# Kernel tuning notes

Hardware: AMD Instinct MI355X
Metric: run time of the kernel (lower is better)

Reference implementation:

```python
import jax, jax.numpy as jnp
import numpy as np

LAYERS = 20
BLOCK = 10
K = 2
LC = 16   # layer channels
SC = 32   # skip channels
AC = 64   # aggregate channels
CLASSES = 256


def causal_conv(x, W, b, dilation):
    # x: (B, Cin, N), W: (Cout, Cin, K) -> (B, Cout, N), left-padded (causal)
    pad = dilation * (W.shape[-1] - 1)
    y = jax.lax.conv_general_dilated(
        x, W, window_strides=(1,), padding=[(pad, 0)],
        rhs_dilation=(dilation,), dimension_numbers=('NCH', 'OIH', 'NCH'))
    return y + b[None, :, None]


def conv1x1(x, W, b):
    # (B,Cin,N) x (Cout,Cin,1) -> (B,Cout,N)
    return jnp.einsum('bcn,oc->bon', x, W[:, :, 0]) + b[None, :, None]


def setup_inputs() -> dict:
    key = jax.random.key(0)
    ks = jax.random.split(key, 16)
    B, N = 8, 32768
    x_int = jax.random.randint(ks[0], (B, N), 0, 32768, dtype=jnp.int32)
    s = 0.1
    return {
        'x_int': x_int,
        'W0': jax.random.normal(ks[1], (LC, 1, K), jnp.float32) * s,
        'b0': jnp.zeros((LC,), jnp.float32),
        'Wf': jax.random.normal(ks[2], (LAYERS - 1, LC, LC, K), jnp.float32) * s,
        'bf': jnp.zeros((LAYERS - 1, LC), jnp.float32),
        'Wg': jax.random.normal(ks[3], (LAYERS - 1, LC, LC, K), jnp.float32) * s,
        'bg': jnp.zeros((LAYERS - 1, LC), jnp.float32),
        'Wskip': jax.random.normal(ks[4], (LAYERS - 1, SC, LC, 1), jnp.float32) * s,
        'bskip': jnp.zeros((LAYERS - 1, SC), jnp.float32),
        'Wagg': jax.random.normal(ks[5], (AC, SC, 1), jnp.float32) * s,
        'bagg': jnp.zeros((AC,), jnp.float32),
        'Wout': jax.random.normal(ks[6], (CLASSES, AC, 1), jnp.float32) * s,
        'bout': jnp.zeros((CLASSES,), jnp.float32),
    }


def reference(x_int, W0, b0, Wf, bf, Wg, bg, Wskip, bskip, Wagg, bagg, Wout, bout):
    B, N = x_int.shape
    # build_layer_input: normalize, shift right by one sample (causal teacher forcing)
    x = x_int.astype(jnp.float32) / (65536.0 / 2.0)
    x = jnp.concatenate([jnp.zeros((B, 1), jnp.float32), x[:, :-1]], axis=1)
    h = x[:, None, :]                                  # (B, 1, N)

    # layer 0: plain causal conv 1 -> 16 channels; residual broadcasts (B,1,N)+(B,16,N)
    out0 = causal_conv(h, W0, b0, 1)
    h = h + out0                                       # (B, 16, N)

    skip_acc = jnp.zeros((B, SC, N), jnp.float32)
    for i in range(LAYERS - 1):
        d = 2 ** ((i + 1) % BLOCK)
        f = jnp.tanh(causal_conv(h, Wf[i], bf[i], d))
        g = jax.nn.sigmoid(causal_conv(h, Wg[i], bg[i], d))
        skip_acc = skip_acc + conv1x1(h, Wskip[i], bskip[i])  # skip taps layer INPUT (per source)
        h = h + f * g                                  # residual

    agg = conv1x1(jax.nn.relu(skip_acc), Wagg, bagg)   # (B, 64, N)
    logits = conv1x1(jax.nn.relu(agg), Wout, bout)     # (B, 256, N)
    # full-length sequences -> mask is all ones; log-softmax over channel dim
    return jax.nn.log_softmax(logits, axis=1)
```

## Files before the change

### kernel.cpp

```cpp
#include <hip/hip_runtime.h>
#include <math.h>
#include <stdint.h>

#define NPOS  32768
#define LOG2N 15
#define BATCH 8
#define TOTAL (BATCH * NPOS)
#define HE    ((size_t)16 * TOTAL)
#define HFE   ((size_t)16 * TOTAL)

typedef __attribute__((ext_vector_type(8))) short    short8v;
typedef __attribute__((ext_vector_type(8))) _Float16 half8v;
typedef __attribute__((ext_vector_type(4))) float    f32x4;

__device__ __forceinline__ float fast_tanh(float x) {
    float t = __expf(-2.f * x);
    return fmaf(2.f, __builtin_amdgcn_rcpf(1.f + t), -1.f);
}
__device__ __forceinline__ float fast_sigmoid(float x) {
    return __builtin_amdgcn_rcpf(1.f + __expf(-x));
}
__device__ __forceinline__ unsigned short bf16rne(float x) {
    unsigned u = __float_as_uint(x);
    u = (u + 0x7fffu + ((u >> 16) & 1u)) >> 16;
    return (unsigned short)u;
}
__device__ __forceinline__ unsigned short f16bits(float x) {
    union { _Float16 h; unsigned short u; } cv;
    cv.h = (_Float16)x;
    return cv.u;
}


__global__ __launch_bounds__(256) void init_f16(
    const int* __restrict__ x_int, const float* __restrict__ W0,
    const float* __restrict__ b0, _Float16* __restrict__ H0)
{
    int t0 = (blockIdx.x * 256 + threadIdx.x) * 2;
    int n0 = t0 & (NPOS - 1);
    const float sc = 1.f / 32768.f;
    float xs0  = (n0 >= 1) ? (float)x_int[t0 - 1] * sc : 0.f;
    float xs1  = (float)x_int[t0] * sc;
    float xsp0 = (n0 >= 2) ? (float)x_int[t0 - 2] * sc : 0.f;
    float xsp1 = xs0;

    half8v o[4];
#pragma unroll
    for (int c = 0; c < 16; ++c) {
        float a = xs0 + W0[c * 2 + 0] * xsp0 + W0[c * 2 + 1] * xs0 + b0[c];
        float b = xs1 + W0[c * 2 + 0] * xsp1 + W0[c * 2 + 1] * xs1 + b0[c];
        o[c >> 3][c & 7]       = (_Float16)a;
        o[2 + (c >> 3)][c & 7] = (_Float16)b;
    }
    half8v* op = (half8v*)(H0 + (size_t)t0 * 16);
    op[0] = o[0]; op[1] = o[1]; op[2] = o[2]; op[3] = o[3];
}

__global__ __launch_bounds__(256, 4) void layer_mfma(
    const _Float16* __restrict__ hIn, _Float16* __restrict__ hOut,
    const float* __restrict__ wf, const float* __restrict__ bfv,
    const float* __restrict__ wg, const float* __restrict__ bgv,
    int d)
{
    const int tid  = threadIdx.x;
    const int lane = tid & 63;
    const int wv   = tid >> 6;
    const int lr   = lane & 15;
    const int lg   = lane >> 4;

    const int koff = (lg & 1) * 8;
    const int sel  = lg >> 1;
    half8v af, ag;
#pragma unroll
    for (int j = 0; j < 8; ++j) {
        af[j] = (_Float16)wf[(lr * 16 + koff + j) * 2 + sel];
        ag[j] = (_Float16)wg[(lr * 16 + koff + j) * 2 + sel];
    }
    f32x4 cf0, cg0;
#pragma unroll
    for (int r = 0; r < 4; ++r) {
        cf0[r] = bfv[lg * 4 + r];
        cg0[r] = bgv[lg * 4 + r];
    }

    const int waveBase = blockIdx.x * 256 + wv * 64;

#pragma unroll
    for (int nt = 0; nt < 4; ++nt) {
        int t = waveBase + nt * 16 + lr;
        int n = t & (NPOS - 1);

        half8v bfr;
        if (sel == 0) {
            bool v = (n >= d);
            const half8v* p = (const half8v*)(hIn + (size_t)(v ? (t - d) : t) * 16 + koff);
            half8v x = *p;
            if (!v) {
#pragma unroll
                for (int j = 0; j < 8; ++j) x[j] = (_Float16)0.f;
            }
            bfr = x;
        } else {
            bfr = *(const half8v*)(hIn + (size_t)t * 16 + koff);
        }

        f32x4 fAcc = __builtin_amdgcn_mfma_f32_16x16x32_f16(af, bfr, cf0, 0, 0, 0);
        f32x4 gAcc = __builtin_amdgcn_mfma_f32_16x16x32_f16(ag, bfr, cg0, 0, 0, 0);

        const _Float16* hold = hIn + (size_t)t * 16 + lg * 4;
        unsigned pk0, pk1;
        {
            float v0 = fmaf(fast_tanh(fAcc[0]), fast_sigmoid(gAcc[0]), (float)hold[0]);
            float v1 = fmaf(fast_tanh(fAcc[1]), fast_sigmoid(gAcc[1]), (float)hold[1]);
            float v2 = fmaf(fast_tanh(fAcc[2]), fast_sigmoid(gAcc[2]), (float)hold[2]);
            float v3 = fmaf(fast_tanh(fAcc[3]), fast_sigmoid(gAcc[3]), (float)hold[3]);
            pk0 = (unsigned)f16bits(v0) | ((unsigned)f16bits(v1) << 16);
            pk1 = (unsigned)f16bits(v2) | ((unsigned)f16bits(v3) << 16);
        }
        *(uint2*)(hOut + (size_t)t * 16 + lg * 4) = make_uint2(pk0, pk1);
    }
}

__global__ __launch_bounds__(256, 2) void final_f16(
    const _Float16* __restrict__ Hf,
    const float* __restrict__ Wsk,  const float* __restrict__ bskv,
    const float* __restrict__ Wagg, const float* __restrict__ bagg,
    const float* __restrict__ Wout, const float* __restrict__ bout,
    float* __restrict__ out)
{
    __shared__ float sv_lds[64][33];
    __shared__ unsigned short agg_bu[64 * 64];
    __shared__ float red_m[64][5];
    __shared__ float red_s[64][5];
    __shared__ float bsum[32];

    int tid  = threadIdx.x;
    int lane = tid & 63;
    int w    = tid >> 6;
    int posG = blockIdx.x * 64;
    int b    = posG >> LOG2N;
    int nb   = posG & (NPOS - 1);

    int lr = lane & 15;
    int lg = lane >> 4;

    if (tid < 32) {
        float s = 0.f;
#pragma unroll 1
        for (int i = 0; i < 19; ++i) s += bskv[i * 32 + tid];
        bsum[tid] = s;
    }

    int posGlob = posG + w * 16 + lr;

    f32x4 dsk0 = {0.f, 0.f, 0.f, 0.f};
    f32x4 dsk1 = {0.f, 0.f, 0.f, 0.f};

#pragma unroll
    for (int kt = 0; kt < 10; ++kt) {
        int i   = kt * 2 + (lg >> 1);
        int ic0 = (lg & 1) * 8;
        half8v bfr = {0, 0, 0, 0, 0, 0, 0, 0};
        half8v af0 = {0, 0, 0, 0, 0, 0, 0, 0};
        half8v af1 = {0, 0, 0, 0, 0, 0, 0, 0};
        if (i < 19) {
            bfr = *(const half8v*)(Hf + (size_t)i * HFE + (size_t)posGlob * 16 + ic0);

            const float4* wp0 = (const float4*)(Wsk + (size_t)i * 512 + (0 * 16 + lr) * 16 + ic0);
            const float4* wp1 = (const float4*)(Wsk + (size_t)i * 512 + (1 * 16 + lr) * 16 + ic0);
            float4 a0 = wp0[0], a1 = wp0[1];
            float4 c0v = wp1[0], c1v = wp1[1];
            af0[0] = (_Float16)a0.x; af0[1] = (_Float16)a0.y;
            af0[2] = (_Float16)a0.z; af0[3] = (_Float16)a0.w;
            af0[4] = (_Float16)a1.x; af0[5] = (_Float16)a1.y;
            af0[6] = (_Float16)a1.z; af0[7] = (_Float16)a1.w;
            af1[0] = (_Float16)c0v.x; af1[1] = (_Float16)c0v.y;
            af1[2] = (_Float16)c0v.z; af1[3] = (_Float16)c0v.w;
            af1[4] = (_Float16)c1v.x; af1[5] = (_Float16)c1v.y;
            af1[6] = (_Float16)c1v.z; af1[7] = (_Float16)c1v.w;
        }
        dsk0 = __builtin_amdgcn_mfma_f32_16x16x32_f16(af0, bfr, dsk0, 0, 0, 0);
        dsk1 = __builtin_amdgcn_mfma_f32_16x16x32_f16(af1, bfr, dsk1, 0, 0, 0);
    }

    __syncthreads();

    {
        int posL = w * 16 + lr;
#pragma unroll
        for (int r = 0; r < 4; ++r) {
            int sc0 = 0 * 16 + lg * 4 + r;
            int sc1 = 1 * 16 + lg * 4 + r;
            sv_lds[posL][sc0] = fmaxf(dsk0[r] + bsum[sc0], 0.f);
            sv_lds[posL][sc1] = fmaxf(dsk1[r] + bsum[sc1], 0.f);
        }
    }
    __syncthreads();

    {
        float sv[32];
#pragma unroll
        for (int sch = 0; sch < 32; ++sch) sv[sch] = sv_lds[lane][sch];

        float r16[16];
#pragma unroll
        for (int a = 0; a < 16; ++a) {
            int ac = w * 16 + a;
            float acc = bagg[ac];
#pragma unroll
            for (int sch = 0; sch < 32; ++sch)
                acc = fmaf(Wagg[ac * 32 + sch], sv[sch], acc);
            r16[a] = fmaxf(acc, 0.f);
        }
#pragma unroll
        for (int q = 0; q < 8; ++q) {
            unsigned pk = (unsigned)f16bits(r16[2 * q]) |
                          ((unsigned)f16bits(r16[2 * q + 1]) << 16);
            int icbyte = (w * 16 + 2 * q) * 2;
            int addr   = lane * 128 + (icbyte ^ ((lane & 7) << 4));
            *(unsigned*)(&agg_bu[addr >> 1]) = pk;
        }
    }
    __syncthreads();

    int c0 = w * 64;
    half8v afr[4][2];
#pragma unroll
    for (int ct = 0; ct < 4; ++ct) {
#pragma unroll
        for (int kf = 0; kf < 2; ++kf) {
            int cls = c0 + ct * 16 + lr;
            int k0  = kf * 32 + lg * 8;
            const float4* wp = (const float4*)(Wout + (size_t)cls * 64 + k0);
            float4 w0 = wp[0], w1 = wp[1];
            half8v af;
            af[0] = (_Float16)w0.x; af[1] = (_Float16)w0.y;
            af[2] = (_Float16)w0.z; af[3] = (_Float16)w0.w;
            af[4] = (_Float16)w1.x; af[5] = (_Float16)w1.y;
            af[6] = (_Float16)w1.z; af[7] = (_Float16)w1.w;
            afr[ct][kf] = af;
        }
    }

    f32x4 acc[4][4];
#pragma unroll
    for (int pt = 0; pt < 4; ++pt) {
        int pos = pt * 16 + lr;
        int sw  = (pos & 7) << 4;
        const half8v* bp0 = (const half8v*)(&agg_bu[(pos * 128 + ((0 * 64 + lg * 16) ^ sw)) >> 1]);
        const half8v* bp1 = (const half8v*)(&agg_bu[(pos * 128 + ((1 * 64 + lg * 16) ^ sw)) >> 1]);
        half8v bf0 = *bp0;
        half8v bf1 = *bp1;
#pragma unroll
        for (int ct = 0; ct < 4; ++ct) {
            f32x4 c;
#pragma unroll
            for (int r = 0; r < 4; ++r) c[r] = bout[c0 + ct * 16 + lg * 4 + r];
            c = __builtin_amdgcn_mfma_f32_16x16x32_f16(afr[ct][0], bf0, c, 0, 0, 0);
            c = __builtin_amdgcn_mfma_f32_16x16x32_f16(afr[ct][1], bf1, c, 0, 0, 0);
            acc[pt][ct] = c;
        }
    }

#pragma unroll
    for (int pt = 0; pt < 4; ++pt) {
        float m = -1e30f;
#pragma unroll
        for (int ct = 0; ct < 4; ++ct)
#pragma unroll
            for (int r = 0; r < 4; ++r) m = fmaxf(m, acc[pt][ct][r]);
        m = fmaxf(m, __shfl_xor(m, 16));
        m = fmaxf(m, __shfl_xor(m, 32));
        float s = 0.f;
#pragma unroll
        for (int ct = 0; ct < 4; ++ct)
#pragma unroll
            for (int r = 0; r < 4; ++r) s += __expf(acc[pt][ct][r] - m);
        s += __shfl_xor(s, 16);
        s += __shfl_xor(s, 32);
        int pos = pt * 16 + lr;
        red_m[pos][w] = m;
        red_s[pos][w] = s;
    }
    __syncthreads();

#pragma unroll
    for (int pt = 0; pt < 4; ++pt) {
        int pos = pt * 16 + lr;
        float M = fmaxf(fmaxf(red_m[pos][0], red_m[pos][1]),
                        fmaxf(red_m[pos][2], red_m[pos][3]));
        float S = 0.f;
#pragma unroll
        for (int k = 0; k < 4; ++k) S += red_s[pos][k] * __expf(red_m[pos][k] - M);
        float logZ = M + __logf(S);

        int n = nb + pos;
#pragma unroll
        for (int ct = 0; ct < 4; ++ct) {
#pragma unroll
            for (int r = 0; r < 4; ++r) {
                int cls = c0 + ct * 16 + lg * 4 + r;
                out[((size_t)(b * 256 + cls)) * NPOS + n] = acc[pt][ct][r] - logZ;
            }
        }
    }
}

__global__ __launch_bounds__(256) void init_kernel2(
    const int* __restrict__ x_int, const float* __restrict__ W0,
    const float* __restrict__ b0, float* __restrict__ h)
{
    int t0 = (blockIdx.x * 256 + threadIdx.x) * 2;
    int n0 = t0 & (NPOS - 1);
    const float sc = 1.f / 32768.f;
    float xs0  = (n0 >= 1) ? (float)x_int[t0 - 1] * sc : 0.f;
    float xs1  = (float)x_int[t0] * sc;
    float xsp0 = (n0 >= 2) ? (float)x_int[t0 - 2] * sc : 0.f;
    float xsp1 = xs0;
#pragma unroll
    for (int c = 0; c < 16; ++c) {
        float2 o;
        o.x = xs0 + W0[c * 2 + 0] * xsp0 + W0[c * 2 + 1] * xs0 + b0[c];
        o.y = xs1 + W0[c * 2 + 0] * xsp1 + W0[c * 2 + 1] * xs1 + b0[c];
        *(float2*)(h + (size_t)c * TOTAL + t0) = o;
    }
}

__global__ __launch_bounds__(256, 2) void layer_kernel2(
    const float* __restrict__ hIn, float* __restrict__ hOut,
    float* __restrict__ skip,
    const float* __restrict__ wf, const float* __restrict__ bfv,
    const float* __restrict__ wg, const float* __restrict__ bgv,
    const float* __restrict__ wsk, const float* __restrict__ bskv,
    int d, int firstLayer)
{
    int t0 = (blockIdx.x * 256 + threadIdx.x) * 2;
    int n0 = t0 & (NPOS - 1);

    float2 hc[16], hp[16];
#pragma unroll
    for (int ic = 0; ic < 16; ++ic)
        hc[ic] = *(const float2*)(hIn + (size_t)ic * TOTAL + t0);

    if (d == 1) {
        bool v = (n0 >= 1);
        int tm = v ? (t0 - 1) : t0;
#pragma unroll
        for (int ic = 0; ic < 16; ++ic) {
            float x = hIn[(size_t)ic * TOTAL + tm];
            hp[ic].x = v ? x : 0.f;
            hp[ic].y = hc[ic].x;
        }
    } else {
        bool v = (n0 >= d);
        int tm = v ? (t0 - d) : t0;
#pragma unroll
        for (int ic = 0; ic < 16; ++ic) {
            float2 x = *(const float2*)(hIn + (size_t)ic * TOTAL + tm);
            hp[ic].x = v ? x.x : 0.f;
            hp[ic].y = v ? x.y : 0.f;
        }
    }

    float2 fa[16], ga[16];
#pragma unroll
    for (int c = 0; c < 16; ++c) {
        fa[c].x = fa[c].y = bfv[c];
        ga[c].x = ga[c].y = bgv[c];
    }
#pragma unroll
    for (int c = 0; c < 16; ++c) {
#pragma unroll
        for (int ic = 0; ic < 16; ++ic) {
            float wf0 = wf[(c * 16 + ic) * 2 + 0];
            float wf1 = wf[(c * 16 + ic) * 2 + 1];
            float wg0 = wg[(c * 16 + ic) * 2 + 0];
            float wg1 = wg[(c * 16 + ic) * 2 + 1];
            fa[c].x = fmaf(wf0, hp[ic].x, fa[c].x);
            fa[c].x = fmaf(wf1, hc[ic].x, fa[c].x);
            fa[c].y = fmaf(wf0, hp[ic].y, fa[c].y);
            fa[c].y = fmaf(wf1, hc[ic].y, fa[c].y);
            ga[c].x = fmaf(wg0, hp[ic].x, ga[c].x);
            ga[c].x = fmaf(wg1, hc[ic].x, ga[c].x);
            ga[c].y = fmaf(wg0, hp[ic].y, ga[c].y);
            ga[c].y = fmaf(wg1, hc[ic].y, ga[c].y);
        }
    }

#pragma unroll
    for (int c = 0; c < 16; ++c) {
        float2 o;
        o.x = fmaf(fast_tanh(fa[c].x), fast_sigmoid(ga[c].x), hc[c].x);
        o.y = fmaf(fast_tanh(fa[c].y), fast_sigmoid(ga[c].y), hc[c].y);
        *(float2*)(hOut + (size_t)c * TOTAL + t0) = o;
    }

#pragma unroll
    for (int sch = 0; sch < 32; ++sch) {
        float2 acc;
        acc.x = acc.y = bskv[sch];
#pragma unroll
        for (int ic = 0; ic < 16; ++ic) {
            float wv = wsk[sch * 16 + ic];
            acc.x = fmaf(wv, hc[ic].x, acc.x);
            acc.y = fmaf(wv, hc[ic].y, acc.y);
        }
        float* sp = skip + (size_t)sch * TOTAL + t0;
        if (firstLayer) {
            *(float2*)sp = acc;
        } else {
            float2 old = *(const float2*)sp;
            acc.x += old.x; acc.y += old.y;
            *(float2*)sp = acc;
        }
    }
}

__global__ __launch_bounds__(256, 2) void final_kernel(
    const float* __restrict__ skip,
    const float* __restrict__ Wagg, const float* __restrict__ bagg,
    const float* __restrict__ Wout, const float* __restrict__ bout,
    float* __restrict__ out)
{
    __shared__ unsigned short agg_bu[64 * 64];
    __shared__ float red_m[64][5];
    __shared__ float red_s[64][5];

    int tid  = threadIdx.x;
    int lane = tid & 63;
    int w    = tid >> 6;
    int posG = blockIdx.x * 64;
    int b    = posG >> LOG2N;
    int nb   = posG & (NPOS - 1);

    {
        int pos = posG + lane;
        float sv[32];
#pragma unroll
        for (int sch = 0; sch < 32; ++sch)
            sv[sch] = fmaxf(skip[(size_t)sch * TOTAL + pos], 0.f);

        float r16[16];
#pragma unroll
        for (int a = 0; a < 16; ++a) {
            int ac = w * 16 + a;
            float acc = bagg[ac];
#pragma unroll
            for (int sch = 0; sch < 32; ++sch)
                acc = fmaf(Wagg[ac * 32 + sch], sv[sch], acc);
            r16[a] = fmaxf(acc, 0.f);
        }
#pragma unroll
        for (int q = 0; q < 8; ++q) {
            unsigned pk = (unsigned)bf16rne(r16[2 * q]) |
                          ((unsigned)bf16rne(r16[2 * q + 1]) << 16);
            int icbyte = (w * 16 + 2 * q) * 2;
            int addr   = lane * 128 + (icbyte ^ ((lane & 7) << 4));
            *(unsigned*)(&agg_bu[addr >> 1]) = pk;
        }
    }
    __syncthreads();

    int lr = lane & 15;
    int lg = lane >> 4;
    int c0 = w * 64;
    short8v afr[4][2];
#pragma unroll
    for (int ct = 0; ct < 4; ++ct) {
#pragma unroll
        for (int kf = 0; kf < 2; ++kf) {
            int cls = c0 + ct * 16 + lr;
            int k0  = kf * 32 + lg * 8;
            const float4* wp = (const float4*)(Wout + (size_t)cls * 64 + k0);
            float4 w0 = wp[0], w1 = wp[1];
            short8v af;
            af[0] = (short)bf16rne(w0.x); af[1] = (short)bf16rne(w0.y);
            af[2] = (short)bf16rne(w0.z); af[3] = (short)bf16rne(w0.w);
            af[4] = (short)bf16rne(w1.x); af[5] = (short)bf16rne(w1.y);
            af[6] = (short)bf16rne(w1.z); af[7] = (short)bf16rne(w1.w);
            afr[ct][kf] = af;
        }
    }

    f32x4 acc[4][4];
#pragma unroll
    for (int pt = 0; pt < 4; ++pt) {
        int pos = pt * 16 + lr;
        int sw  = (pos & 7) << 4;
        const short8v* bp0 = (const short8v*)(&agg_bu[(pos * 128 + ((0 * 64 + lg * 16) ^ sw)) >> 1]);
        const short8v* bp1 = (const short8v*)(&agg_bu[(pos * 128 + ((1 * 64 + lg * 16) ^ sw)) >> 1]);
        short8v bf0 = *bp0;
        short8v bf1 = *bp1;
#pragma unroll
        for (int ct = 0; ct < 4; ++ct) {
            f32x4 c;
#pragma unroll
            for (int r = 0; r < 4; ++r) c[r] = bout[c0 + ct * 16 + lg * 4 + r];
            c = __builtin_amdgcn_mfma_f32_16x16x32_bf16(afr[ct][0], bf0, c, 0, 0, 0);
            c = __builtin_amdgcn_mfma_f32_16x16x32_bf16(afr[ct][1], bf1, c, 0, 0, 0);
            acc[pt][ct] = c;
        }
    }

#pragma unroll
    for (int pt = 0; pt < 4; ++pt) {
        float m = -1e30f;
#pragma unroll
        for (int ct = 0; ct < 4; ++ct)
#pragma unroll
            for (int r = 0; r < 4; ++r) m = fmaxf(m, acc[pt][ct][r]);
        m = fmaxf(m, __shfl_xor(m, 16));
        m = fmaxf(m, __shfl_xor(m, 32));
        float s = 0.f;
#pragma unroll
        for (int ct = 0; ct < 4; ++ct)
#pragma unroll
            for (int r = 0; r < 4; ++r) s += __expf(acc[pt][ct][r] - m);
        s += __shfl_xor(s, 16);
        s += __shfl_xor(s, 32);
        int pos = pt * 16 + lr;
        red_m[pos][w] = m;
        red_s[pos][w] = s;
    }
    __syncthreads();

#pragma unroll
    for (int pt = 0; pt < 4; ++pt) {
        int pos = pt * 16 + lr;
        float M = fmaxf(fmaxf(red_m[pos][0], red_m[pos][1]),
                        fmaxf(red_m[pos][2], red_m[pos][3]));
        float S = 0.f;
#pragma unroll
        for (int k = 0; k < 4; ++k) S += red_s[pos][k] * __expf(red_m[pos][k] - M);
        float logZ = M + __logf(S);

        int n = nb + pos;
#pragma unroll
        for (int ct = 0; ct < 4; ++ct) {
#pragma unroll
            for (int r = 0; r < 4; ++r) {
                int cls = c0 + ct * 16 + lg * 4 + r;
                out[((size_t)(b * 256 + cls)) * NPOS + n] = acc[pt][ct][r] - logZ;
            }
        }
    }
}

extern "C" void kernel_launch(void* const* d_in, const int* in_sizes, int n_in,
                              void* d_out, int out_size, void* d_ws, size_t ws_size,
                              hipStream_t stream)
{
    const int*   x_int = (const int*)  d_in[0];
    const float* W0    = (const float*)d_in[1];
    const float* b0    = (const float*)d_in[2];
    const float* Wf    = (const float*)d_in[3];
    const float* bfv   = (const float*)d_in[4];
    const float* Wg    = (const float*)d_in[5];
    const float* bgv   = (const float*)d_in[6];
    const float* Wsk   = (const float*)d_in[7];
    const float* bskv  = (const float*)d_in[8];
    const float* Wagg  = (const float*)d_in[9];
    const float* bagg  = (const float*)d_in[10];
    const float* Wout  = (const float*)d_in[11];
    const float* bout  = (const float*)d_in[12];
    float* out = (float*)d_out;

    const size_t needF16 = 19 * HFE * sizeof(_Float16);
    const int grid2 = TOTAL / (256 * 2);

    if (ws_size >= needF16) {
        _Float16* Hf = (_Float16*)d_ws;

        init_f16<<<grid2, 256, 0, stream>>>(x_int, W0, b0, Hf);
        for (int i = 0; i < 18; ++i) {
            int d = 1 << ((i + 1) % 10);
            layer_mfma<<<TOTAL / 256, 256, 0, stream>>>(
                Hf + (size_t)i * HFE, Hf + (size_t)(i + 1) * HFE,
                Wf + (size_t)i * 512, bfv + (size_t)i * 16,
                Wg + (size_t)i * 512, bgv + (size_t)i * 16, d);
        }
        final_f16<<<TOTAL / 64, 256, 0, stream>>>(
            Hf, Wsk, bskv, Wagg, bagg, Wout, bout, out);
    } else {
        const size_t skE = (size_t)32 * TOTAL;
        float* skipb = (float*)d_ws;
        float *hA, *hB;
        if (ws_size >= (skE + 2 * HE) * sizeof(float)) {
            hA = skipb + skE;
            hB = hA + HE;
        } else {
            hA = out + ((size_t)out_size - 2 * HE);
            hB = hA + HE;
        }

        init_kernel2<<<grid2, 256, 0, stream>>>(x_int, W0, b0, hA);
        float* hin = hA;
        float* hout = hB;
        for (int i = 0; i < 19; ++i) {
            int d = 1 << ((i + 1) % 10);
            layer_kernel2<<<grid2, 256, 0, stream>>>(
                hin, hout, skipb,
                Wf + (size_t)i * 512, bfv + (size_t)i * 16,
                Wg + (size_t)i * 512, bgv + (size_t)i * 16,
                Wsk + (size_t)i * 512, bskv + (size_t)i * 32,
                d, (i == 0) ? 1 : 0);
            float* tmp = hin; hin = hout; hout = tmp;
        }
        final_kernel<<<TOTAL / 64, 256, 0, stream>>>(
            skipb, Wagg, bagg, Wout, bout, out);
    }
}
```

Before: 435.7 us.

## Fuse consecutive gated residual layers pairwise with LDS halo recompute

Replaces the per-layer MFMA kernel with a kernel that computes two consecutive dilated layers in one launch. Layer A is computed over the block's 256 positions plus a left halo rounded up from layer B's dilation, and its output is kept in shared memory. Layer B then reads from shared memory instead of re-reading layer A's output from global memory. Layer A's output is still written to global memory because the final kernel needs every layer's hidden state. This halves the number of layer launches and cuts one global read per pair, at the cost of recomputing halo positions (up to double work for large dilations) and a block-wide barrier.

```diff
diff --git a/kernel.cpp b/kernel.cpp
--- a/kernel.cpp
+++ b/kernel.cpp
@@ -11,6 +11,7 @@
 
 typedef __attribute__((ext_vector_type(8))) short    short8v;
 typedef __attribute__((ext_vector_type(8))) _Float16 half8v;
+typedef __attribute__((ext_vector_type(4))) _Float16 half4v;
 typedef __attribute__((ext_vector_type(4))) float    f32x4;
 
 __device__ __forceinline__ float fast_tanh(float x) {
@@ -56,68 +57,117 @@
     op[0] = o[0]; op[1] = o[1]; op[2] = o[2]; op[3] = o[3];
 }
 
-__global__ __launch_bounds__(256, 4) void layer_mfma(
-    const _Float16* __restrict__ hIn, _Float16* __restrict__ hOut,
-    const float* __restrict__ wf, const float* __restrict__ bfv,
-    const float* __restrict__ wg, const float* __restrict__ bgv,
-    int d)
+__global__ __launch_bounds__(256, 4) void pair_mfma(
+    const _Float16* __restrict__ hIn,
+    _Float16* __restrict__ hAout, _Float16* __restrict__ hBout,
+    const float* __restrict__ wfA, const float* __restrict__ bfA,
+    const float* __restrict__ wgA, const float* __restrict__ bgA,
+    const float* __restrict__ wfB, const float* __restrict__ bfB,
+    const float* __restrict__ wgB, const float* __restrict__ bgB,
+    int dA, int dB, int haloR)
 {
+    __shared__ _Float16 mid[512][16];
+
     const int tid  = threadIdx.x;
     const int lane = tid & 63;
     const int wv   = tid >> 6;
     const int lr   = lane & 15;
     const int lg   = lane >> 4;
-
     const int koff = (lg & 1) * 8;
     const int sel  = lg >> 1;
-    half8v af, ag;
+
+    const int base  = blockIdx.x * 256;
+    const int tiles = (256 + haloR) >> 4;
+
+    half8v afA, agA;
 #pragma unroll
     for (int j = 0; j < 8; ++j) {
-        af[j] = (_Float16)wf[(lr * 16 + koff + j) * 2 + sel];
-        ag[j] = (_Float16)wg[(lr * 16 + koff + j) * 2 + sel];
-    }
-    f32x4 cf0, cg0;
-#pragma unroll
-    for (int r = 0; r < 4; ++r) {
-        cf0[r] = bfv[lg * 4 + r];
-        cg0[r] = bgv[lg * 4 + r];
-    }
-
-    const int waveBase = blockIdx.x * 256 + wv * 64;
-
-#pragma unroll
-    for (int nt = 0; nt < 4; ++nt) {
-        int t = waveBase + nt * 16 + lr;
-        int n = t & (NPOS - 1);
+        afA[j] = (_Float16)wfA[(lr * 16 + koff + j) * 2 + sel];
+        agA[j] = (_Float16)wgA[(lr * 16 + koff + j) * 2 + sel];
+    }
+    f32x4 cfA, cgA;
+#pragma unroll
+    for (int r = 0; r < 4; ++r) { cfA[r] = bfA[lg * 4 + r]; cgA[r] = bgA[lg * 4 + r]; }
+
+#pragma unroll 1
+    for (int tt = wv; tt < tiles; tt += 4) {
+        int loc0 = tt * 16;
+        int t  = base - haloR + loc0 + lr;
+        int tc = (t < 0) ? 0 : t;
+        int n  = t & (NPOS - 1);
 
         half8v bfr;
         if (sel == 0) {
-            bool v = (n >= d);
-            const half8v* p = (const half8v*)(hIn + (size_t)(v ? (t - d) : t) * 16 + koff);
-            half8v x = *p;
+            bool v = (t >= 0) && (n >= dA);
+            half8v x = *(const half8v*)(hIn + (size_t)(v ? (t - dA) : tc) * 16 + koff);
             if (!v) {
 #pragma unroll
                 for (int j = 0; j < 8; ++j) x[j] = (_Float16)0.f;
             }
             bfr = x;
         } else {
-            bfr = *(const half8v*)(hIn + (size_t)t * 16 + koff);
-        }
-
-        f32x4 fAcc = __builtin_amdgcn_mfma_f32_16x16x32_f16(af, bfr, cf0, 0, 0, 0);
-        f32x4 gAcc = __builtin_amdgcn_mfma_f32_16x16x32_f16(ag, bfr, cg0, 0, 0, 0);
-
-        const _Float16* hold = hIn + (size_t)t * 16 + lg * 4;
-        unsigned pk0, pk1;
+            bfr = *(const half8v*)(hIn + (size_t)tc * 16 + koff);
+        }
+
+        f32x4 fAcc = __builtin_amdgcn_mfma_f32_16x16x32_f16(afA, bfr, cfA, 0, 0, 0);
+        f32x4 gAcc = __builtin_amdgcn_mfma_f32_16x16x32_f16(agA, bfr, cgA, 0, 0, 0);
+
+        const _Float16* hold = hIn + (size_t)tc * 16 + lg * 4;
+        half4v w4;
         {
-            float v0 = fmaf(fast_tanh(fAcc[0]), fast_sigmoid(gAcc[0]), (float)hold[0]);
-            float v1 = fmaf(fast_tanh(fAcc[1]), fast_sigmoid(gAcc[1]), (float)hold[1]);
-            float v2 = fmaf(fast_tanh(fAcc[2]), fast_sigmoid(gAcc[2]), (float)hold[2]);
-            float v3 = fmaf(fast_tanh(fAcc[3]), fast_sigmoid(gAcc[3]), (float)hold[3]);
-            pk0 = (unsigned)f16bits(v0) | ((unsigned)f16bits(v1) << 16);
-            pk1 = (unsigned)f16bits(v2) | ((unsigned)f16bits(v3) << 16);
-        }
-        *(uint2*)(hOut + (size_t)t * 16 + lg * 4) = make_uint2(pk0, pk1);
+            w4[0] = (_Float16)fmaf(fast_tanh(fAcc[0]), fast_sigmoid(gAcc[0]), (float)hold[0]);
+            w4[1] = (_Float16)fmaf(fast_tanh(fAcc[1]), fast_sigmoid(gAcc[1]), (float)hold[1]);
+            w4[2] = (_Float16)fmaf(fast_tanh(fAcc[2]), fast_sigmoid(gAcc[2]), (float)hold[2]);
+            w4[3] = (_Float16)fmaf(fast_tanh(fAcc[3]), fast_sigmoid(gAcc[3]), (float)hold[3]);
+        }
+        *(half4v*)(&mid[loc0 + lr][lg * 4]) = w4;
+        if (t >= 0)
+            *(half4v*)(hAout + (size_t)t * 16 + lg * 4) = w4;
+    }
+    __syncthreads();
+
+    half8v afB, agB;
+#pragma unroll
+    for (int j = 0; j < 8; ++j) {
+        afB[j] = (_Float16)wfB[(lr * 16 + koff + j) * 2 + sel];
+        agB[j] = (_Float16)wgB[(lr * 16 + koff + j) * 2 + sel];
+    }
+    f32x4 cfB, cgB;
+#pragma unroll
+    for (int r = 0; r < 4; ++r) { cfB[r] = bfB[lg * 4 + r]; cgB[r] = bgB[lg * 4 + r]; }
+
+#pragma unroll
+    for (int nt = 0; nt < 4; ++nt) {
+        int local0 = wv * 64 + nt * 16;
+        int t   = base + local0 + lr;
+        int n   = t & (NPOS - 1);
+        int loc = haloR + local0 + lr;
+
+        half8v bfr;
+        if (sel == 0) {
+            bool v = (n >= dB);
+            half8v x = *(const half8v*)(&mid[v ? (loc - dB) : loc][koff]);
+            if (!v) {
+#pragma unroll
+                for (int j = 0; j < 8; ++j) x[j] = (_Float16)0.f;
+            }
+            bfr = x;
+        } else {
+            bfr = *(const half8v*)(&mid[loc][koff]);
+        }
+
+        f32x4 fAcc = __builtin_amdgcn_mfma_f32_16x16x32_f16(afB, bfr, cfB, 0, 0, 0);
+        f32x4 gAcc = __builtin_amdgcn_mfma_f32_16x16x32_f16(agB, bfr, cgB, 0, 0, 0);
+
+        const _Float16* hold = &mid[loc][lg * 4];
+        half4v w4;
+        {
+            w4[0] = (_Float16)fmaf(fast_tanh(fAcc[0]), fast_sigmoid(gAcc[0]), (float)hold[0]);
+            w4[1] = (_Float16)fmaf(fast_tanh(fAcc[1]), fast_sigmoid(gAcc[1]), (float)hold[1]);
+            w4[2] = (_Float16)fmaf(fast_tanh(fAcc[2]), fast_sigmoid(gAcc[2]), (float)hold[2]);
+            w4[3] = (_Float16)fmaf(fast_tanh(fAcc[3]), fast_sigmoid(gAcc[3]), (float)hold[3]);
+        }
+        *(half4v*)(hBout + (size_t)t * 16 + lg * 4) = w4;
     }
 }
 
@@ -572,12 +622,19 @@
         _Float16* Hf = (_Float16*)d_ws;
 
         init_f16<<<grid2, 256, 0, stream>>>(x_int, W0, b0, Hf);
-        for (int i = 0; i < 18; ++i) {
-            int d = 1 << ((i + 1) % 10);
-            layer_mfma<<<TOTAL / 256, 256, 0, stream>>>(
-                Hf + (size_t)i * HFE, Hf + (size_t)(i + 1) * HFE,
-                Wf + (size_t)i * 512, bfv + (size_t)i * 16,
-                Wg + (size_t)i * 512, bgv + (size_t)i * 16, d);
+        for (int p = 0; p < 9; ++p) {
+            int iA = 2 * p, iB = 2 * p + 1;
+            int dA = 1 << ((iA + 1) % 10);
+            int dB = 1 << ((iB + 1) % 10);
+            int haloR = (dB + 15) & ~15;
+            pair_mfma<<<TOTAL / 256, 256, 0, stream>>>(
+                Hf + (size_t)iA * HFE,
+                Hf + (size_t)(iA + 1) * HFE, Hf + (size_t)(iB + 1) * HFE,
+                Wf + (size_t)iA * 512, bfv + (size_t)iA * 16,
+                Wg + (size_t)iA * 512, bgv + (size_t)iA * 16,
+                Wf + (size_t)iB * 512, bfv + (size_t)iB * 16,
+                Wg + (size_t)iB * 512, bgv + (size_t)iB * 16,
+                dA, dB, haloR);
         }
         final_f16<<<TOTAL / 64, 256, 0, stream>>>(
             Hf, Wsk, bskv, Wagg, bagg, Wout, bout, out);
```

Measured after the change: 414.1 us. 1.05x faster.

## Fuse groups of dilated layers into one kernel with LDS halo tiles

Applied to the files above, without the earlier changes.

Replaces 18 per-layer launches with 4 grouped launches, each computing up to 5 consecutive layers per 256-position tile. The intermediate h values are kept in shared memory, and the causal halo region is recomputed from the left. Only the snapshots needed by the final skip kernel are written to global memory. This cuts launch count and global reads of h, at the cost of redundant halo computation, a __syncthreads per chunk, and LDS capacity limits on occupancy.

```diff
diff --git a/kernel.cpp b/kernel.cpp
--- a/kernel.cpp
+++ b/kernel.cpp
@@ -8,9 +8,11 @@
 #define TOTAL (BATCH * NPOS)
 #define HE    ((size_t)16 * TOTAL)
 #define HFE   ((size_t)16 * TOTAL)
+#define WMAX  736
 
 typedef __attribute__((ext_vector_type(8))) short    short8v;
 typedef __attribute__((ext_vector_type(8))) _Float16 half8v;
+typedef __attribute__((ext_vector_type(4))) _Float16 half4v;
 typedef __attribute__((ext_vector_type(4))) float    f32x4;
 
 __device__ __forceinline__ float fast_tanh(float x) {
@@ -56,68 +58,114 @@
     op[0] = o[0]; op[1] = o[1]; op[2] = o[2]; op[3] = o[3];
 }
 
-__global__ __launch_bounds__(256, 4) void layer_mfma(
-    const _Float16* __restrict__ hIn, _Float16* __restrict__ hOut,
-    const float* __restrict__ wf, const float* __restrict__ bfv,
-    const float* __restrict__ wg, const float* __restrict__ bgv,
-    int d)
+__global__ __launch_bounds__(256, 4) void group_mfma(
+    const _Float16* __restrict__ hIn, _Float16* __restrict__ Hbase,
+    const float* __restrict__ Wf, const float* __restrict__ bfv,
+    const float* __restrict__ Wg, const float* __restrict__ bgv,
+    int iStart, int L)
 {
+    __shared__ _Float16 mid[WMAX * 16];
+
     const int tid  = threadIdx.x;
     const int lane = tid & 63;
     const int wv   = tid >> 6;
     const int lr   = lane & 15;
     const int lg   = lane >> 4;
-
     const int koff = (lg & 1) * 8;
     const int sel  = lg >> 1;
-    half8v af, ag;
-#pragma unroll
-    for (int j = 0; j < 8; ++j) {
-        af[j] = (_Float16)wf[(lr * 16 + koff + j) * 2 + sel];
-        ag[j] = (_Float16)wg[(lr * 16 + koff + j) * 2 + sel];
-    }
-    f32x4 cf0, cg0;
-#pragma unroll
-    for (int r = 0; r < 4; ++r) {
-        cf0[r] = bfv[lg * 4 + r];
-        cg0[r] = bgv[lg * 4 + r];
-    }
-
-    const int waveBase = blockIdx.x * 256 + wv * 64;
-
-#pragma unroll
-    for (int nt = 0; nt < 4; ++nt) {
-        int t = waveBase + nt * 16 + lr;
-        int n = t & (NPOS - 1);
-
-        half8v bfr;
-        if (sel == 0) {
-            bool v = (n >= d);
-            const half8v* p = (const half8v*)(hIn + (size_t)(v ? (t - d) : t) * 16 + koff);
-            half8v x = *p;
-            if (!v) {
-#pragma unroll
-                for (int j = 0; j < 8; ++j) x[j] = (_Float16)0.f;
+
+    int X[5];
+    X[0] = 0;
+    for (int k = 1; k < L; ++k) {
+        int dk = 1 << ((iStart + k + 1) % 10);
+        X[k] = (X[k - 1] + dk + 15) & ~15;
+    }
+    const int Hlo = X[L - 1];
+    const int W   = 256 + Hlo;
+    const int base = blockIdx.x * 256;
+
+#pragma unroll 1
+    for (int k = 0; k < L; ++k) {
+        const int i = iStart + k;
+        const int d = 1 << ((i + 1) % 10);
+        const float* wfL = Wf + (size_t)i * 512;
+        const float* wgL = Wg + (size_t)i * 512;
+        const float* bfL = bfv + i * 16;
+        const float* bgL = bgv + i * 16;
+        _Float16* snap = Hbase + (size_t)(i + 1) * HFE;
+
+        half8v af, ag;
+#pragma unroll
+        for (int j = 0; j < 8; ++j) {
+            af[j] = (_Float16)wfL[(lr * 16 + koff + j) * 2 + sel];
+            ag[j] = (_Float16)wgL[(lr * 16 + koff + j) * 2 + sel];
+        }
+        f32x4 cf, cg;
+#pragma unroll
+        for (int r = 0; r < 4; ++r) { cf[r] = bfL[lg * 4 + r]; cg[r] = bgL[lg * 4 + r]; }
+
+        const int xlo = X[k];
+        const int nch = (W - xlo + 63) >> 6;
+
+#pragma unroll 1
+        for (int c = 0; c < nch; ++c) {
+            int x0 = W - (c + 1) * 64 + wv * 16;
+            bool act = (x0 >= xlo);
+            int x = x0 + lr;
+            int t = base - Hlo + x;
+            int n = t & (NPOS - 1);
+
+            half4v w4;
+            if (act) {
+                half8v bfr;
+                half4v holdv;
+                if (k == 0) {
+                    int tc = (t < 0) ? 0 : t;
+                    if (sel == 0) {
+                        bool v = (t >= 0) && (n >= d);
+                        half8v xv = *(const half8v*)(hIn + (size_t)(v ? (t - d) : tc) * 16 + koff);
+                        if (!v) {
+#pragma unroll
+                            for (int j = 0; j < 8; ++j) xv[j] = (_Float16)0.f;
+                        }
+                        bfr = xv;
+                    } else {
+                        bfr = *(const half8v*)(hIn + (size_t)tc * 16 + koff);
+                    }
+                    holdv = *(const half4v*)(hIn + (size_t)tc * 16 + lg * 4);
+                } else {
+                    if (sel == 0) {
+                        bool v = (n >= d);
+                        half8v xv = *(const half8v*)(&mid[(v ? (x - d) : x) * 16 + koff]);
+                        if (!v) {
+#pragma unroll
+                            for (int j = 0; j < 8; ++j) xv[j] = (_Float16)0.f;
+                        }
+                        bfr = xv;
+                    } else {
+                        bfr = *(const half8v*)(&mid[x * 16 + koff]);
+                    }
+                    holdv = *(const half4v*)(&mid[x * 16 + lg * 4]);
+                }
+
+                f32x4 fAcc = __builtin_amdgcn_mfma_f32_16x16x32_f16(af, bfr, cf, 0, 0, 0);
+                f32x4 gAcc = __builtin_amdgcn_mfma_f32_16x16x32_f16(ag, bfr, cg, 0, 0, 0);
+
+                w4[0] = (_Float16)fmaf(fast_tanh(fAcc[0]), fast_sigmoid(gAcc[0]), (float)holdv[0]);
+                w4[1] = (_Float16)fmaf(fast_tanh(fAcc[1]), fast_sigmoid(gAcc[1]), (float)holdv[1]);
+                w4[2] = (_Float16)fmaf(fast_tanh(fAcc[2]), fast_sigmoid(gAcc[2]), (float)holdv[2]);
+                w4[3] = (_Float16)fmaf(fast_tanh(fAcc[3]), fast_sigmoid(gAcc[3]), (float)holdv[3]);
             }
-            bfr = x;
-        } else {
-            bfr = *(const half8v*)(hIn + (size_t)t * 16 + koff);
-        }
-
-        f32x4 fAcc = __builtin_amdgcn_mfma_f32_16x16x32_f16(af, bfr, cf0, 0, 0, 0);
-        f32x4 gAcc = __builtin_amdgcn_mfma_f32_16x16x32_f16(ag, bfr, cg0, 0, 0, 0);
-
-        const _Float16* hold = hIn + (size_t)t * 16 + lg * 4;
-        unsigned pk0, pk1;
-        {
-            float v0 = fmaf(fast_tanh(fAcc[0]), fast_sigmoid(gAcc[0]), (float)hold[0]);
-            float v1 = fmaf(fast_tanh(fAcc[1]), fast_sigmoid(gAcc[1]), (float)hold[1]);
-            float v2 = fmaf(fast_tanh(fAcc[2]), fast_sigmoid(gAcc[2]), (float)hold[2]);
-            float v3 = fmaf(fast_tanh(fAcc[3]), fast_sigmoid(gAcc[3]), (float)hold[3]);
-            pk0 = (unsigned)f16bits(v0) | ((unsigned)f16bits(v1) << 16);
-            pk1 = (unsigned)f16bits(v2) | ((unsigned)f16bits(v3) << 16);
-        }
-        *(uint2*)(hOut + (size_t)t * 16 + lg * 4) = make_uint2(pk0, pk1);
+
+            __syncthreads();
+
+            if (act) {
+                *(half4v*)(&mid[x * 16 + lg * 4]) = w4;
+                if (x0 >= Hlo)
+                    *(half4v*)(snap + (size_t)t * 16 + lg * 4) = w4;
+            }
+        }
+        __syncthreads();
     }
 }
 
@@ -572,12 +620,13 @@
         _Float16* Hf = (_Float16*)d_ws;
 
         init_f16<<<grid2, 256, 0, stream>>>(x_int, W0, b0, Hf);
-        for (int i = 0; i < 18; ++i) {
-            int d = 1 << ((i + 1) % 10);
-            layer_mfma<<<TOTAL / 256, 256, 0, stream>>>(
-                Hf + (size_t)i * HFE, Hf + (size_t)(i + 1) * HFE,
-                Wf + (size_t)i * 512, bfv + (size_t)i * 16,
-                Wg + (size_t)i * 512, bgv + (size_t)i * 16, d);
+
+        const int gs[4] = {0, 5, 8, 13};
+        const int gl[4] = {5, 3, 5, 5};
+        for (int g = 0; g < 4; ++g) {
+            group_mfma<<<TOTAL / 256, 256, 0, stream>>>(
+                Hf + (size_t)gs[g] * HFE, Hf,
+                Wf, bfv, Wg, bgv, gs[g], gl[g]);
         }
         final_f16<<<TOTAL / 64, 256, 0, stream>>>(
             Hf, Wsk, bskv, Wagg, bagg, Wout, bout, out);
```

New measurement: 416.1 us. -4.5%, faster.
